# Optimization experiments

Hardware: AMD Instinct MI355X
Metric: run time of the kernel (lower is better)

Reference implementation:

```python
import jax, jax.numpy as jnp
import numpy as np

EPS = 1e-3  # tf.keras.layers.BatchNormalization default epsilon


def setup_inputs() -> dict:
    key = jax.random.key(0)
    k1, k2 = jax.random.split(key)
    B, N, F = 16, 8192, 256
    voxel_features = jax.random.normal(k1, (B, N, F), dtype=jnp.float32)
    num_valid_voxels = jax.random.randint(k2, (B,), 0, N, dtype=jnp.int32)
    gamma = jnp.ones((F,), dtype=jnp.float32)
    beta = jnp.zeros((F,), dtype=jnp.float32)
    return {
        "voxel_features": voxel_features,
        "num_valid_voxels": num_valid_voxels,
        "gamma": gamma,
        "beta": beta,
    }


def reference(voxel_features, num_valid_voxels, gamma, beta):
    # voxel_features: [B, N, F]; num_valid_voxels: [B]
    B, N, F = voxel_features.shape
    # mask[b, n] = n < num_valid_voxels[b]
    mask = (jnp.arange(N, dtype=jnp.int32)[None, :] < num_valid_voxels[:, None])
    maskf = mask.astype(voxel_features.dtype)[:, :, None]  # [B, N, 1]
    count = jnp.maximum(jnp.sum(num_valid_voxels).astype(voxel_features.dtype), 1.0)
    xm = voxel_features * maskf
    # Batch statistics over valid voxels only (per-feature), biased variance as BN uses
    mean = jnp.sum(xm, axis=(0, 1)) / count                      # [F]
    var = jnp.sum((voxel_features - mean) ** 2 * maskf, axis=(0, 1)) / count  # [F]
    inv_std = jax.lax.rsqrt(var + EPS)
    normed = (voxel_features - mean) * inv_std * gamma + beta
    # Padding positions are zeroed (the original pads unpadded outputs with zeros)
    return normed * maskf
```

## Files before the change

kernel.cpp:

```cpp
#include <hip/hip_runtime.h>

#define Bdim 16
#define Ndim 8192
#define Fdim 256
#define EPS 1e-3f

#define RED_BLOCKS 512
#define NORM_BLOCKS 2048
#define TOTAL_CHUNKS (Bdim * Ndim * (Fdim / 4))
#define NORM_ITERS (TOTAL_CHUNKS / (NORM_BLOCKS * 256))

typedef float fx4 __attribute__((ext_vector_type(4)));


__global__ __launch_bounds__(512) void init_kernel(float* __restrict__ ws) {
    ws[threadIdx.x] = 0.0f;
}

__global__ __launch_bounds__(256) void reduce_kernel(
    const float* __restrict__ x, const int* __restrict__ nv,
    float* __restrict__ ws)
{
    __shared__ float lds_s[4][Fdim];
    __shared__ float lds_q[4][Fdim];
    __shared__ int s_pre[Bdim + 1];
    const int tid = threadIdx.x;
    if (tid == 0) {
        int acc = 0;
        s_pre[0] = 0;
        #pragma unroll
        for (int i = 0; i < Bdim; i++) { acc += nv[i]; s_pre[i + 1] = acc; }
    }
    __syncthreads();

    const int V = s_pre[Bdim];
    const int per = V / RED_BLOCKS, rem = V % RED_BLOCKS;
    const int g = blockIdx.x;
    const int k0 = g * per + (g < rem ? g : rem);
    const int kE = k0 + per + (g < rem ? 1 : 0);

    const int c = tid & 63;
    const int r = tid >> 6;
    const fx4* xc = (const fx4*)x + c;

    float s0=0.f,s1=0.f,s2=0.f,s3=0.f, q0=0.f,q1=0.f,q2=0.f,q3=0.f;

    int k = k0 + r;
    int b = 0, pre_b = 0, pre_next = s_pre[1];
    if (k < kE) {
        while (k >= pre_next) { ++b; pre_b = pre_next; pre_next = s_pre[b + 1]; }
    }

    #define ROW_OF(kk, rowvar)                                                  \
        while ((kk) >= pre_next) { ++b; pre_b = pre_next; pre_next = s_pre[b+1]; } \
        const int rowvar = (b << 13) + ((kk) - pre_b);

    for (; k + 12 < kE; k += 16) {
        ROW_OF(k,      row0)
        ROW_OF(k + 4,  row1)
        ROW_OF(k + 8,  row2)
        ROW_OF(k + 12, row3)
        const fx4 v0 = xc[(size_t)row0 * 64];
        const fx4 v1 = xc[(size_t)row1 * 64];
        const fx4 v2 = xc[(size_t)row2 * 64];
        const fx4 v3 = xc[(size_t)row3 * 64];
        s0 += v0.x; q0 += v0.x*v0.x;  s1 += v0.y; q1 += v0.y*v0.y;
        s2 += v0.z; q2 += v0.z*v0.z;  s3 += v0.w; q3 += v0.w*v0.w;
        s0 += v1.x; q0 += v1.x*v1.x;  s1 += v1.y; q1 += v1.y*v1.y;
        s2 += v1.z; q2 += v1.z*v1.z;  s3 += v1.w; q3 += v1.w*v1.w;
        s0 += v2.x; q0 += v2.x*v2.x;  s1 += v2.y; q1 += v2.y*v2.y;
        s2 += v2.z; q2 += v2.z*v2.z;  s3 += v2.w; q3 += v2.w*v2.w;
        s0 += v3.x; q0 += v3.x*v3.x;  s1 += v3.y; q1 += v3.y*v3.y;
        s2 += v3.z; q2 += v3.z*v3.z;  s3 += v3.w; q3 += v3.w*v3.w;
    }
    for (; k < kE; k += 4) {
        ROW_OF(k, row)
        const fx4 v = xc[(size_t)row * 64];
        s0 += v.x; q0 += v.x*v.x;  s1 += v.y; q1 += v.y*v.y;
        s2 += v.z; q2 += v.z*v.z;  s3 += v.w; q3 += v.w*v.w;
    }
    #undef ROW_OF

    const int f0 = c * 4;
    lds_s[r][f0+0]=s0; lds_s[r][f0+1]=s1; lds_s[r][f0+2]=s2; lds_s[r][f0+3]=s3;
    lds_q[r][f0+0]=q0; lds_q[r][f0+1]=q1; lds_q[r][f0+2]=q2; lds_q[r][f0+3]=q3;
    __syncthreads();

    float ts = 0.0f, tq = 0.0f;
    #pragma unroll
    for (int rr = 0; rr < 4; rr++) { ts += lds_s[rr][tid]; tq += lds_q[rr][tid]; }
    unsafeAtomicAdd(&ws[tid], ts);
    unsafeAtomicAdd(&ws[Fdim + tid], tq);
}

__global__ __launch_bounds__(256) void norm_kernel(
    const float* __restrict__ x, const int* __restrict__ nv,
    const float* __restrict__ gamma, const float* __restrict__ beta,
    const float* __restrict__ ws, float* __restrict__ out)
{
    __shared__ float s_sc[Fdim], s_bi[Fdim];
    __shared__ int s_nv[Bdim];
    const int tid = threadIdx.x;
    if (tid < Bdim) s_nv[tid] = nv[tid];
    __syncthreads();
    {
        int cnt = 0;
        #pragma unroll
        for (int i = 0; i < Bdim; i++) cnt += s_nv[i];
        const float inv_count = 1.0f / fmaxf((float)cnt, 1.0f);
        const float mean = ws[tid] * inv_count;
        float var = fmaf(ws[Fdim + tid], inv_count, -mean * mean);
        var = fmaxf(var, 0.0f);
        const float s = rsqrtf(var + EPS) * gamma[tid];
        s_sc[tid] = s;
        s_bi[tid] = fmaf(-mean, s, beta[tid]);
    }
    __syncthreads();

    const int c = tid & 63;
    const fx4 sc = ((const fx4*)s_sc)[c];
    const fx4 bi = ((const fx4*)s_bi)[c];

    const int base = blockIdx.x * 256 + tid;
    const int stride = NORM_BLOCKS * 256;
    #pragma unroll
    for (int it = 0; it < NORM_ITERS; it++) {
        const int idx = base + it * stride;
        const int row = idx >> 6;
        const int b = row >> 13;
        const int n = row & (Ndim - 1);
        fx4* po = (fx4*)out + idx;
        if (n < s_nv[b]) {
            const fx4 v = ((const fx4*)x)[idx];
            fx4 o;
            o.x = fmaf(v.x, sc.x, bi.x);
            o.y = fmaf(v.y, sc.y, bi.y);
            o.z = fmaf(v.z, sc.z, bi.z);
            o.w = fmaf(v.w, sc.w, bi.w);
            __builtin_nontemporal_store(o, po);
        } else {
            const fx4 z = {0.f, 0.f, 0.f, 0.f};
            __builtin_nontemporal_store(z, po);
        }
    }
}

extern "C" void kernel_launch(void* const* d_in, const int* in_sizes, int n_in,
                              void* d_out, int out_size, void* d_ws, size_t ws_size,
                              hipStream_t stream) {
    const float* x     = (const float*)d_in[0];
    const int*   nv    = (const int*)d_in[1];
    const float* gamma = (const float*)d_in[2];
    const float* beta  = (const float*)d_in[3];
    float* out = (float*)d_out;
    float* ws  = (float*)d_ws;

    init_kernel<<<1, 512, 0, stream>>>(ws);
    reduce_kernel<<<RED_BLOCKS, 256, 0, stream>>>(x, nv, ws);
    norm_kernel<<<NORM_BLOCKS, 256, 0, stream>>>(x, nv, gamma, beta, ws, out);
}
```

Measured before the change: 236.6 us.

## Fuse init, reduce and normalize into one cooperative kernel with grid syncs

Merges the three kernel launches into one cooperative kernel of 1024 blocks that zeroes the workspace, syncs the grid, accumulates per-feature sum and sum of squares with atomics, syncs again, then normalizes. This removes the separate launches and the gaps between kernels. The cost is two grid-wide barriers and fewer blocks for the streaming normalize pass (1024 blocks with 4 per SM, partial unroll), which may lower memory-level parallelism. Cooperative launch also needs the whole grid to be resident at once.

```diff
diff --git a/kernel.cpp b/kernel.cpp
--- a/kernel.cpp
+++ b/kernel.cpp
@@ -1,30 +1,34 @@
 #include <hip/hip_runtime.h>
+#include <hip/hip_cooperative_groups.h>
+
+namespace cg = cooperative_groups;
 
 #define Bdim 16
 #define Ndim 8192
 #define Fdim 256
 #define EPS 1e-3f
 
-#define RED_BLOCKS 512
-#define NORM_BLOCKS 2048
+#define BLOCKS 1024
 #define TOTAL_CHUNKS (Bdim * Ndim * (Fdim / 4))
-#define NORM_ITERS (TOTAL_CHUNKS / (NORM_BLOCKS * 256))
+#define NORM_ITERS (TOTAL_CHUNKS / (BLOCKS * 256))
 
 typedef float fx4 __attribute__((ext_vector_type(4)));
 
+__global__ __launch_bounds__(256, 4) void fused_kernel(
+    const float* __restrict__ x, const int* __restrict__ nv,
+    const float* __restrict__ gamma, const float* __restrict__ beta,
+    float* __restrict__ ws, float* __restrict__ out)
+{
+    cg::grid_group grid = cg::this_grid();
+    const int tid = threadIdx.x;
+    const int g = blockIdx.x;
 
-__global__ __launch_bounds__(512) void init_kernel(float* __restrict__ ws) {
-    ws[threadIdx.x] = 0.0f;
-}
+    if (g < 2) ws[g * 256 + tid] = 0.0f;
 
-__global__ __launch_bounds__(256) void reduce_kernel(
-    const float* __restrict__ x, const int* __restrict__ nv,
-    float* __restrict__ ws)
-{
+    __shared__ int s_pre[Bdim + 1];
     __shared__ float lds_s[4][Fdim];
     __shared__ float lds_q[4][Fdim];
-    __shared__ int s_pre[Bdim + 1];
-    const int tid = threadIdx.x;
+    __shared__ float s_sc[Fdim], s_bi[Fdim];
     if (tid == 0) {
         int acc = 0;
         s_pre[0] = 0;
@@ -33,9 +37,10 @@
     }
     __syncthreads();
 
+    grid.sync();
+
     const int V = s_pre[Bdim];
-    const int per = V / RED_BLOCKS, rem = V % RED_BLOCKS;
-    const int g = blockIdx.x;
+    const int per = V / BLOCKS, rem = V % BLOCKS;
     const int k0 = g * per + (g < rem ? g : rem);
     const int kE = k0 + per + (g < rem ? 1 : 0);
 
@@ -51,7 +56,7 @@
         while (k >= pre_next) { ++b; pre_b = pre_next; pre_next = s_pre[b + 1]; }
     }
 
-    #define ROW_OF(kk, rowvar)                                                  \
+    #define ROW_OF(kk, rowvar)                                                     \
         while ((kk) >= pre_next) { ++b; pre_b = pre_next; pre_next = s_pre[b+1]; } \
         const int rowvar = (b << 13) + ((kk) - pre_b);
 
@@ -86,28 +91,18 @@
     lds_q[r][f0+0]=q0; lds_q[r][f0+1]=q1; lds_q[r][f0+2]=q2; lds_q[r][f0+3]=q3;
     __syncthreads();
 
-    float ts = 0.0f, tq = 0.0f;
-    #pragma unroll
-    for (int rr = 0; rr < 4; rr++) { ts += lds_s[rr][tid]; tq += lds_q[rr][tid]; }
-    unsafeAtomicAdd(&ws[tid], ts);
-    unsafeAtomicAdd(&ws[Fdim + tid], tq);
-}
+    {
+        float ts = 0.0f, tq = 0.0f;
+        #pragma unroll
+        for (int rr = 0; rr < 4; rr++) { ts += lds_s[rr][tid]; tq += lds_q[rr][tid]; }
+        unsafeAtomicAdd(&ws[tid], ts);
+        unsafeAtomicAdd(&ws[Fdim + tid], tq);
+    }
 
-__global__ __launch_bounds__(256) void norm_kernel(
-    const float* __restrict__ x, const int* __restrict__ nv,
-    const float* __restrict__ gamma, const float* __restrict__ beta,
-    const float* __restrict__ ws, float* __restrict__ out)
-{
-    __shared__ float s_sc[Fdim], s_bi[Fdim];
-    __shared__ int s_nv[Bdim];
-    const int tid = threadIdx.x;
-    if (tid < Bdim) s_nv[tid] = nv[tid];
-    __syncthreads();
+    grid.sync();
+
     {
-        int cnt = 0;
-        #pragma unroll
-        for (int i = 0; i < Bdim; i++) cnt += s_nv[i];
-        const float inv_count = 1.0f / fmaxf((float)cnt, 1.0f);
+        const float inv_count = 1.0f / fmaxf((float)V, 1.0f);
         const float mean = ws[tid] * inv_count;
         float var = fmaf(ws[Fdim + tid], inv_count, -mean * mean);
         var = fmaxf(var, 0.0f);
@@ -117,20 +112,19 @@
     }
     __syncthreads();
 
-    const int c = tid & 63;
     const fx4 sc = ((const fx4*)s_sc)[c];
     const fx4 bi = ((const fx4*)s_bi)[c];
 
-    const int base = blockIdx.x * 256 + tid;
-    const int stride = NORM_BLOCKS * 256;
-    #pragma unroll
+    const int base = g * 256 + tid;
+    const int stride = BLOCKS * 256;
+    #pragma unroll 4
     for (int it = 0; it < NORM_ITERS; it++) {
         const int idx = base + it * stride;
         const int row = idx >> 6;
-        const int b = row >> 13;
+        const int bb = row >> 13;
         const int n = row & (Ndim - 1);
         fx4* po = (fx4*)out + idx;
-        if (n < s_nv[b]) {
+        if (n < s_pre[bb + 1] - s_pre[bb]) {
             const fx4 v = ((const fx4*)x)[idx];
             fx4 o;
             o.x = fmaf(v.x, sc.x, bi.x);
@@ -155,7 +149,8 @@
     float* out = (float*)d_out;
     float* ws  = (float*)d_ws;
 
-    init_kernel<<<1, 512, 0, stream>>>(ws);
-    reduce_kernel<<<RED_BLOCKS, 256, 0, stream>>>(x, nv, ws);
-    norm_kernel<<<NORM_BLOCKS, 256, 0, stream>>>(x, nv, gamma, beta, ws, out);
+    void* args[] = {(void*)&x, (void*)&nv, (void*)&gamma, (void*)&beta,
+                    (void*)&ws, (void*)&out};
+    hipLaunchCooperativeKernel((const void*)fused_kernel,
+                               dim3(BLOCKS), dim3(256), args, 0, stream);
 }
```

Result: slower. 382.8 us (+61.8%).
